# Kernel tuning notes

Measured on AMD Instinct MI355X. Metric: run time of the kernel, lower is better.

The kernel has to match this reference:

```python
import jax, jax.numpy as jnp
import numpy as np

D = 256   # hidden_dim
N = 1024  # total nodes
NP = 384  # paratope nodes
NE = 384  # epitope nodes
NC = 14   # atom channels


def setup_inputs() -> dict:
    key = jax.random.key(0)
    ks = jax.random.split(key, 24)
    s = 1.0 / np.sqrt(D)
    s3 = 1.0 / np.sqrt(3 * D)
    w = lambda k, shape, sc: (jax.random.normal(k, shape, jnp.float32) * sc)
    z = lambda: jnp.zeros((D,), jnp.float32)
    return {
        "H": w(ks[0], (N, D), 1.0),
        "X": w(ks[1], (N, NC, 3), 1.0),
        "paratope_mask": jnp.zeros((N,), bool).at[:NP].set(True),
        "epitope_mask": jnp.zeros((N,), bool).at[NP:NP + NE].set(True),
        "res_w1": w(ks[2], (1, D), 1.0), "res_b1": z(),
        "res_w2": w(ks[3], (D, D), s), "res_b2": z(),
        "atom_w1": w(ks[4], (1, D), 1.0), "atom_b1": z(),
        "atom_w2": w(ks[5], (D, D), s), "atom_b2": z(),
        "sim_weight": jnp.float32(0.5),
        "int_w1": w(ks[6], (3 * D, D), s3), "int_b1": z(),
        "int_w2": w(ks[7], (D, D), s), "int_b2": z(),
        "wl": w(ks[8], (D, D), s),
        "wr": w(ks[9], (D, D), s),
        "wg_w": w(ks[10], (D, D), s), "wg_b": z(),
        "wq_w": w(ks[11], (D, D), s), "wq_b": z(),
        "wk_w": w(ks[12], (D, D), s), "wk_b": z(),
        "wv_w": w(ks[13], (D, D), s), "wv_b": z(),
    }


def _mlp2(x, w1, b1, w2, b2):
    return jax.nn.silu(x @ w1 + b1) @ w2 + b2


def reference(H, X, paratope_mask, epitope_mask,
              res_w1, res_b1, res_w2, res_b2,
              atom_w1, atom_b1, atom_w2, atom_b2,
              sim_weight,
              int_w1, int_b1, int_w2, int_b2,
              wl, wr, wg_w, wg_b, wq_w, wq_b, wk_w, wk_b, wv_w, wv_b):
    p_idx = jnp.nonzero(paratope_mask, size=NP)[0]
    e_idx = jnp.nonzero(epitope_mask, size=NE)[0]
    Hp = H[p_idx]                      # [NP, D]
    He = H[e_idx]                      # [NE, D]
    Xp_ca = X[p_idx, 1]                # [NP, 3] (CA atom)
    Xe_ca = X[e_idx, 1]                # [NE, 3]

    dX = Xp_ca[:, None, :] - Xe_ca[None, :, :]         # [NP, NE, 3]
    S = jnp.sum(dX * dX, axis=-1, keepdims=True)       # [NP, NE, 1]
    # original computes S_residue and S_atom with identical formula
    S_res = _mlp2(S, res_w1, res_b1, res_w2, res_b2)
    S_atom = _mlp2(S, atom_w1, atom_b1, atom_w2, atom_b2)
    wmix = jax.nn.sigmoid(sim_weight)
    S_comb = wmix * S_res + (1.0 - wmix) * S_atom      # [NP, NE, D]

    Hp_e = jnp.broadcast_to(Hp[:, None, :], (NP, NE, D))
    He_e = jnp.broadcast_to(He[None, :, :], (NP, NE, D))
    Z_in = jnp.concatenate([Hp_e, He_e, S_comb], axis=-1)  # [NP, NE, 3D]
    Z = _mlp2(Z_in, int_w1, int_b1, int_w2, int_b2)        # [NP, NE, D]

    I = (Hp @ wl)[:, None, :] * (He @ wr)[None, :, :]      # outer-product interaction
    gate = jax.nn.sigmoid(Z @ wg_w + wg_b)
    f_tri = gate * I

    Q = Z @ wq_w + wq_b
    K = Z @ wk_w + wk_b
    V = Z @ wv_w + wv_b
    scores = jnp.einsum('ped,pfd->pef', Q, K) / (D ** 0.5)  # [NP, NE, NE]
    A = jax.nn.softmax(scores, axis=-1)
    f_att = jnp.einsum('pef,pfd->ped', A, V)

    H_tri = f_tri + f_att                                   # [NP, NE, D]
    return H.at[p_idx].set(H_tri.mean(axis=1))
```

## Files before the change

### kernel.cpp

```cpp
#include <hip/hip_runtime.h>

#define NPAR 384
#define NEPI 384
#define DD   256
#define NTAB 4096
#define SMAX 96.0f
#define SDELTA (SMAX / NTAB)
#define SINVD (NTAB / SMAX)

using bf16x8 = __bf16 __attribute__((ext_vector_type(8)));
using bf16x2 = __bf16 __attribute__((ext_vector_type(2)));
using f32x4  = float __attribute__((ext_vector_type(4)));

#if defined(__has_builtin)
#if __has_builtin(__builtin_amdgcn_cvt_pk_bf16_f32)
#define HAVE_PK_BF16 1
#endif
#endif

__device__ __forceinline__ float sigm(float x) { return 1.0f / (1.0f + __expf(-x)); }
__device__ __forceinline__ float silu(float x) { return x / (1.0f + __expf(-x)); }
__device__ __forceinline__ unsigned short f2bf(float f) {
  unsigned u = __float_as_uint(f);
  u += 0x7fffu + ((u >> 16) & 1u);
  return (unsigned short)(u >> 16);
}
__device__ __forceinline__ float bf2f(unsigned u16) {
  return __uint_as_float(u16 << 16);
}
__device__ __forceinline__ float bf2f_lo(unsigned w) {
  return __uint_as_float(w << 16);
}
__device__ __forceinline__ float bf2f_hi(unsigned w) {
  return __uint_as_float(w & 0xffff0000u);
}
__device__ __forceinline__ uint2 pack4(float a, float b, float c, float d) {
  uint2 r;
#ifdef HAVE_PK_BF16
  bf16x2 lo = __builtin_amdgcn_cvt_pk_bf16_f32(a, b);
  bf16x2 hi = __builtin_amdgcn_cvt_pk_bf16_f32(c, d);
  r.x = __builtin_bit_cast(unsigned, lo);
  r.y = __builtin_bit_cast(unsigned, hi);
#else
  r.x = (unsigned)f2bf(a) | ((unsigned)f2bf(b) << 16);
  r.y = (unsigned)f2bf(c) | ((unsigned)f2bf(d) << 16);
#endif
  return r;
}


__global__ void prep_kernel(
    const float* __restrict__ H, const float* __restrict__ wl,
    const float* __restrict__ wr, const float* __restrict__ int_w1,
    const float* __restrict__ res_w2, const float* __restrict__ atom_w2,
    const float* __restrict__ res_b2, const float* __restrict__ atom_b2,
    const float* __restrict__ int_b1, const float* __restrict__ simw,
    const float* __restrict__ wq_b, const float* __restrict__ wk_w,
    const float* __restrict__ wq_w,
    float* __restrict__ Hpl, float* __restrict__ Her,
    float* __restrict__ P1, float* __restrict__ P2,
    float* __restrict__ MrF, float* __restrict__ MaF,
    float* __restrict__ cvec, float* __restrict__ gv,
    float* __restrict__ WqkF) {
  __shared__ float sbuf[1024];
  const int b = blockIdx.x, t = threadIdx.x;
  if (b < 256) {
    const bool isMa = b >= 128;
    const int i0 = (b & 127) * 2;
    const float wmix = 1.0f / (1.0f + __expf(-simw[0]));
    const float sc = isMa ? (1.0f - wmix) : wmix;
    const float* W2 = isMa ? atom_w2 : res_w2;
    sbuf[t] = W2[i0 * 256 + t];
    sbuf[256 + t] = W2[(i0 + 1) * 256 + t];
    __syncthreads();
    float a0 = 0.f, a1 = 0.f;
#pragma unroll 8
    for (int k = 0; k < 256; ++k) {
      const float w = int_w1[(512 + k) * 256 + t];
      a0 = fmaf(sbuf[k], w, a0);
      a1 = fmaf(sbuf[256 + k], w, a1);
    }
    float* dst = isMa ? MaF : MrF;
    dst[i0 * 256 + t] = a0 * sc;
    dst[(i0 + 1) * 256 + t] = a1 * sc;
  } else if (b == 256) {
    const float wmix = 1.0f / (1.0f + __expf(-simw[0]));
    float acc = int_b1[t];
#pragma unroll 8
    for (int k = 0; k < 256; ++k) {
      float bm = wmix * res_b2[k] + (1.0f - wmix) * atom_b2[k];
      acc += bm * int_w1[(512 + k) * 256 + t];
    }
    cvec[t] = acc;
  } else if (b < 321) {
    const int lane = t & 63, w = t >> 6;
    const int d = (b - 257) * 4 + w;
    float acc = 0.f;
#pragma unroll
    for (int i = 0; i < 4; ++i) {
      const int c = i * 64 + lane;
      acc += wk_w[d * 256 + c] * wq_b[c];
    }
    acc += __shfl_xor(acc, 1);
    acc += __shfl_xor(acc, 2);
    acc += __shfl_xor(acc, 4);
    acc += __shfl_xor(acc, 8);
    acc += __shfl_xor(acc, 16);
    acc += __shfl_xor(acc, 32);
    if (lane == 0) gv[d] = acc;
  } else if (b < 577) {
    const int r = b - 321;
    sbuf[t] = wq_w[r * 256 + t];
    __syncthreads();
    const float* wkrow = wk_w + t * 256;
    float a0 = 0.f, a1 = 0.f, a2 = 0.f, a3 = 0.f;
#pragma unroll 4
    for (int k = 0; k < 256; k += 4) {
      const f32x4 wv4 = *reinterpret_cast<const f32x4*>(&wkrow[k]);
      a0 = fmaf(sbuf[k + 0], wv4[0], a0);
      a1 = fmaf(sbuf[k + 1], wv4[1], a1);
      a2 = fmaf(sbuf[k + 2], wv4[2], a2);
      a3 = fmaf(sbuf[k + 3], wv4[3], a3);
    }
    WqkF[r * 256 + t] = (a0 + a1) + (a2 + a3);
  } else {
    const int idx = b - 577;
    const int seg = idx / 96, r0 = (idx % 96) * 4;
    const float* A;
    const float* B;
    float* C;
    switch (seg) {
      case 0:  A = H + r0 * 256;            B = wl;              C = Hpl + r0 * 256; break;
      case 1:  A = H + (NPAR + r0) * 256;   B = wr;              C = Her + r0 * 256; break;
      case 2:  A = H + r0 * 256;            B = int_w1;          C = P1 + r0 * 256;  break;
      default: A = H + (NPAR + r0) * 256;   B = int_w1 + 65536;  C = P2 + r0 * 256;  break;
    }
#pragma unroll
    for (int j = 0; j < 4; ++j) sbuf[j * 256 + t] = A[j * 256 + t];
    __syncthreads();
    float a0 = 0.f, a1 = 0.f, a2 = 0.f, a3 = 0.f;
#pragma unroll 8
    for (int k = 0; k < 256; ++k) {
      const float bv = B[k * 256 + t];
      a0 = fmaf(sbuf[k], bv, a0);
      a1 = fmaf(sbuf[256 + k], bv, a1);
      a2 = fmaf(sbuf[512 + k], bv, a2);
      a3 = fmaf(sbuf[768 + k], bv, a3);
    }
    C[t] = a0;
    C[256 + t] = a1;
    C[512 + t] = a2;
    C[768 + t] = a3;
  }
}

__global__ void pack_kernel(const float* __restrict__ MrF, const float* __restrict__ MaF,
                            const float* __restrict__ w2, const float* __restrict__ wg,
                            const float* __restrict__ WqkF, unsigned short* __restrict__ wpack) {
  const int idx = blockIdx.x * 256 + threadIdx.x;
  const int m = idx >> 16;
  const int r = idx & 65535;
  const int chunk = r >> 9;
  const int lane = (r >> 3) & 63;
  const int j = r & 7;
  const int k = (chunk >> 4) * 32 + (lane >> 4) * 8 + j;
  const int n = (chunk & 15) * 16 + (lane & 15);
  const float* src;
  switch (m) {
    case 0: src = MrF; break;
    case 1: src = MaF; break;
    case 2: src = w2; break;
    case 3: src = wg; break;
    default: src = WqkF; break;
  }
  wpack[idx] = f2bf(src[k * 256 + n]);
}


__device__ __forceinline__ void zero_acc4(f32x4 (&acc)[4][4]) {
#pragma unroll
  for (int mt = 0; mt < 4; ++mt)
#pragma unroll
    for (int nt = 0; nt < 4; ++nt)
      acc[mt][nt] = (f32x4){0.f, 0.f, 0.f, 0.f};
}

__device__ __forceinline__ void gemm4(f32x4 (&acc)[4][4],
                                      const unsigned short* __restrict__ wp,
                                      const unsigned short* ub, int lane, int wv) {
  const int l15 = lane & 15, l4 = lane >> 4;
#pragma unroll
  for (int ks = 0; ks < 8; ++ks) {
    bf16x8 a[4];
#pragma unroll
    for (int mt = 0; mt < 4; ++mt)
      a[mt] = *reinterpret_cast<const bf16x8*>(wp + ((ks * 16 + wv * 4 + mt) * 64 + lane) * 8);
#pragma unroll
    for (int nt = 0; nt < 4; ++nt) {
      bf16x8 b = *reinterpret_cast<const bf16x8*>(ub + (nt * 16 + l15) * 264 + ks * 32 + l4 * 8);
#pragma unroll
      for (int mt = 0; mt < 4; ++mt)
        acc[mt][nt] = __builtin_amdgcn_mfma_f32_16x16x32_bf16(a[mt], b, acc[mt][nt], 0, 0, 0);
    }
  }
}

__device__ __forceinline__ void fill_u(unsigned short* ub, const float* Sv,
                                       const float* __restrict__ w1,
                                       const float* __restrict__ b1, int t) {
  const int dg = t & 31, rb = t >> 5;
  const f32x4 w1a = *reinterpret_cast<const f32x4*>(&w1[dg * 8]);
  const f32x4 w1b = *reinterpret_cast<const f32x4*>(&w1[dg * 8 + 4]);
  const f32x4 b1a = *reinterpret_cast<const f32x4*>(&b1[dg * 8]);
  const f32x4 b1b = *reinterpret_cast<const f32x4*>(&b1[dg * 8 + 4]);
#pragma unroll
  for (int i = 0; i < 8; ++i) {
    const int e = rb + i * 8;
    const float s = Sv[e];
    uint2 lo = pack4(silu(fmaf(s, w1a[0], b1a[0])), silu(fmaf(s, w1a[1], b1a[1])),
                     silu(fmaf(s, w1a[2], b1a[2])), silu(fmaf(s, w1a[3], b1a[3])));
    uint2 hi = pack4(silu(fmaf(s, w1b[0], b1b[0])), silu(fmaf(s, w1b[1], b1b[1])),
                     silu(fmaf(s, w1b[2], b1b[2])), silu(fmaf(s, w1b[3], b1b[3])));
    uint4 pk = {lo.x, lo.y, hi.x, hi.y};
    *reinterpret_cast<uint4*>(&ub[e * 264 + dg * 8]) = pk;
  }
}


__global__ __launch_bounds__(256, 3) void tab_kernel(
    const float* __restrict__ res_w1, const float* __restrict__ res_b1,
    const float* __restrict__ atom_w1, const float* __restrict__ atom_b1,
    const unsigned short* __restrict__ wpack, unsigned short* __restrict__ tab) {
  __shared__ __align__(16) unsigned short ubuf[64 * 264];
  __shared__ float Sv[64];
  const int t = threadIdx.x, lane = t & 63, wv = t >> 6;
  const int l15 = lane & 15, l4 = lane >> 4;
  const int n0 = blockIdx.x * 64;
  if (t < 64) Sv[t] = (n0 + t) * SDELTA;
  __syncthreads();
  f32x4 acc[4][4];
  zero_acc4(acc);
  fill_u(ubuf, Sv, res_w1, res_b1, t);
  __syncthreads();
  gemm4(acc, wpack + 0 * 65536, ubuf, lane, wv);
  __syncthreads();
  fill_u(ubuf, Sv, atom_w1, atom_b1, t);
  __syncthreads();
  gemm4(acc, wpack + 1 * 65536, ubuf, lane, wv);
#pragma unroll
  for (int mt = 0; mt < 4; ++mt) {
    const int d = wv * 64 + mt * 16 + l4 * 4;
#pragma unroll
    for (int nt = 0; nt < 4; ++nt) {
      const int n = n0 + nt * 16 + l15;
      *reinterpret_cast<uint2*>(&tab[n * 256 + d]) =
          pack4(acc[mt][nt][0], acc[mt][nt][1], acc[mt][nt][2], acc[mt][nt][3]);
    }
  }
}


__global__ __launch_bounds__(256, 4) void pair_kernel(
    const float* __restrict__ Xg, const unsigned short* __restrict__ tab,
    const float* __restrict__ int_b2, const float* __restrict__ wg_b,
    const unsigned short* __restrict__ wpack, const float* __restrict__ cvec,
    const float* __restrict__ P1, const float* __restrict__ P2,
    const float* __restrict__ Hpl, const float* __restrict__ Her,
    float* __restrict__ ftri, unsigned short* __restrict__ Zsw) {
  __shared__ __align__(16) unsigned short ubuf[64 * 264];
  __shared__ float Sv[64];
  __shared__ float pc[DD];
  const int t = threadIdx.x, lane = t & 63, wv = t >> 6;
  const int l15 = lane & 15, l4 = lane >> 4;
  const int p = blockIdx.x / 6, cc = blockIdx.x % 6, e0 = cc * 64;
  const int d0 = wv * 64;

  if (t < 64) {
    const int e = e0 + t;
    float dx = Xg[p * 42 + 3] - Xg[(NPAR + e) * 42 + 3];
    float dy = Xg[p * 42 + 4] - Xg[(NPAR + e) * 42 + 4];
    float dz = Xg[p * 42 + 5] - Xg[(NPAR + e) * 42 + 5];
    Sv[t] = dx * dx + dy * dy + dz * dz;
  }
  pc[t] = P1[p * DD + t] + cvec[t];
  __syncthreads();

  {
    const int dg = t & 31, rb = t >> 5;
    const f32x4 pca = *reinterpret_cast<const f32x4*>(&pc[dg * 8]);
    const f32x4 pcb = *reinterpret_cast<const f32x4*>(&pc[dg * 8 + 4]);
#pragma unroll
    for (int i = 0; i < 8; ++i) {
      const int e = rb + i * 8;
      float sv = Sv[e] * SINVD;
      int idx = (int)sv;
      idx = idx > (NTAB - 2) ? (NTAB - 2) : idx;
      const float fr = sv - (float)idx;
      const uint4 t0 = *reinterpret_cast<const uint4*>(&tab[idx * 256 + dg * 8]);
      const uint4 t1 = *reinterpret_cast<const uint4*>(&tab[(idx + 1) * 256 + dg * 8]);
      const f32x4 p2a = *reinterpret_cast<const f32x4*>(&P2[(e0 + e) * DD + dg * 8]);
      const f32x4 p2b = *reinterpret_cast<const f32x4*>(&P2[(e0 + e) * DD + dg * 8 + 4]);
      float z0 = bf2f_lo(t0.x), z1 = bf2f_hi(t0.x), z2 = bf2f_lo(t0.y), z3 = bf2f_hi(t0.y);
      float z4 = bf2f_lo(t0.z), z5 = bf2f_hi(t0.z), z6 = bf2f_lo(t0.w), z7 = bf2f_hi(t0.w);
      z0 = fmaf(fr, bf2f_lo(t1.x) - z0, z0) + pca[0] + p2a[0];
      z1 = fmaf(fr, bf2f_hi(t1.x) - z1, z1) + pca[1] + p2a[1];
      z2 = fmaf(fr, bf2f_lo(t1.y) - z2, z2) + pca[2] + p2a[2];
      z3 = fmaf(fr, bf2f_hi(t1.y) - z3, z3) + pca[3] + p2a[3];
      z4 = fmaf(fr, bf2f_lo(t1.z) - z4, z4) + pcb[0] + p2b[0];
      z5 = fmaf(fr, bf2f_hi(t1.z) - z5, z5) + pcb[1] + p2b[1];
      z6 = fmaf(fr, bf2f_lo(t1.w) - z6, z6) + pcb[2] + p2b[2];
      z7 = fmaf(fr, bf2f_hi(t1.w) - z7, z7) + pcb[3] + p2b[3];
      uint2 lo = pack4(silu(z0), silu(z1), silu(z2), silu(z3));
      uint2 hi = pack4(silu(z4), silu(z5), silu(z6), silu(z7));
      uint4 pk = {lo.x, lo.y, hi.x, hi.y};
      *reinterpret_cast<uint4*>(&ubuf[e * 264 + dg * 8]) = pk;
    }
  }
  __syncthreads();

  f32x4 acc[4][4];
  zero_acc4(acc);
  gemm4(acc, wpack + 2 * 65536, ubuf, lane, wv);
  __syncthreads();
#pragma unroll
  for (int mt = 0; mt < 4; ++mt) {
    const int d = d0 + mt * 16 + l4 * 4;
    const f32x4 bb = *reinterpret_cast<const f32x4*>(&int_b2[d]);
#pragma unroll
    for (int nt = 0; nt < 4; ++nt) {
      const int e = nt * 16 + l15;
      *reinterpret_cast<uint2*>(&ubuf[e * 264 + d]) =
          pack4(acc[mt][nt][0] + bb[0], acc[mt][nt][1] + bb[1],
                acc[mt][nt][2] + bb[2], acc[mt][nt][3] + bb[3]);
    }
  }
  __syncthreads();

  {
    unsigned short* Zd = Zsw + (size_t)p * 98304 + (size_t)(cc * 4 + wv) * 4096 + lane * 8;
#pragma unroll
    for (int ks = 0; ks < 8; ++ks) {
      *reinterpret_cast<uint4*>(Zd + ks * 512) =
          *reinterpret_cast<const uint4*>(&ubuf[(wv * 16 + l15) * 264 + ks * 32 + l4 * 8]);
    }
  }

  zero_acc4(acc);
  gemm4(acc, wpack + 3 * 65536, ubuf, lane, wv);
#pragma unroll
  for (int mt = 0; mt < 4; ++mt) {
    const int d = d0 + mt * 16 + l4 * 4;
    const f32x4 bb = *reinterpret_cast<const f32x4*>(&wg_b[d]);
    const f32x4 hl = *reinterpret_cast<const f32x4*>(&Hpl[p * DD + d]);
    f32x4 fs = (f32x4){0.f, 0.f, 0.f, 0.f};
#pragma unroll
    for (int nt = 0; nt < 4; ++nt) {
      const int e = e0 + nt * 16 + l15;
      const f32x4 hr = *reinterpret_cast<const f32x4*>(&Her[e * DD + d]);
#pragma unroll
      for (int r = 0; r < 4; ++r)
        fs[r] += sigm(acc[mt][nt][r] + bb[r]) * hr[r];
    }
#pragma unroll
    for (int r = 0; r < 4; ++r) {
      float v = fs[r] * hl[r];
      v += __shfl_xor(v, 1);
      v += __shfl_xor(v, 2);
      v += __shfl_xor(v, 4);
      v += __shfl_xor(v, 8);
      if (l15 == 0) atomicAdd(&ftri[p * DD + d + r], v);
    }
  }
}


__global__ __launch_bounds__(256, 4) void attn_kernel(
    const unsigned short* __restrict__ Zsw, const float* __restrict__ gv,
    const unsigned short* __restrict__ wpack, float* __restrict__ cbufg) {
  __shared__ __align__(16) unsigned short Tc[32 * 264];
  __shared__ float red[128];
  __shared__ float red2[128];
  const int t = threadIdx.x, lane = t & 63, wv = t >> 6;
  const int l15 = lane & 15, l4 = lane >> 4;
  const int xcd = blockIdx.x & 7, inner = blockIdx.x >> 3;
  const int p = (inner / 12) * 8 + xcd, c = inner % 12;
  const unsigned short* Zsp = Zsw + (size_t)p * 98304;
  const unsigned short* wqk = wpack + 4 * 65536;

  {
    f32x4 ta[4][2];
#pragma unroll
    for (int mt = 0; mt < 4; ++mt)
#pragma unroll
      for (int nt = 0; nt < 2; ++nt) ta[mt][nt] = (f32x4){0.f, 0.f, 0.f, 0.f};
    const unsigned short* Tb = Zsp + (size_t)(c * 2) * 4096 + lane * 8;
    bf16x8 bcur[2], bnxt[2];
#pragma unroll
    for (int nt = 0; nt < 2; ++nt)
      bcur[nt] = *reinterpret_cast<const bf16x8*>(Tb + nt * 4096);
#pragma unroll
    for (int ks = 0; ks < 8; ++ks) {
      if (ks < 7) {
#pragma unroll
        for (int nt = 0; nt < 2; ++nt)
          bnxt[nt] = *reinterpret_cast<const bf16x8*>(Tb + nt * 4096 + (ks + 1) * 512);
      }
      bf16x8 a[4];
#pragma unroll
      for (int mt = 0; mt < 4; ++mt)
        a[mt] = *reinterpret_cast<const bf16x8*>(wqk + ((ks * 16 + wv * 4 + mt) * 64 + lane) * 8);
#pragma unroll
      for (int nt = 0; nt < 2; ++nt)
#pragma unroll
        for (int mt = 0; mt < 4; ++mt)
          ta[mt][nt] = __builtin_amdgcn_mfma_f32_16x16x32_bf16(a[mt], bcur[nt], ta[mt][nt], 0, 0, 0);
      if (ks < 7) {
#pragma unroll
        for (int nt = 0; nt < 2; ++nt) bcur[nt] = bnxt[nt];
      }
    }
#pragma unroll
    for (int mt = 0; mt < 4; ++mt) {
      const int d = wv * 64 + mt * 16 + l4 * 4;
      const f32x4 gq = *reinterpret_cast<const f32x4*>(&gv[d]);
#pragma unroll
      for (int nt = 0; nt < 2; ++nt) {
        const int e = nt * 16 + l15;
        *reinterpret_cast<uint2*>(&Tc[e * 264 + d]) =
            pack4((ta[mt][nt][0] + gq[0]) * 0.0625f, (ta[mt][nt][1] + gq[1]) * 0.0625f,
                  (ta[mt][nt][2] + gq[2]) * 0.0625f, (ta[mt][nt][3] + gq[3]) * 0.0625f);
      }
    }
  }
  __syncthreads();

  f32x4 sc[2][6];
#pragma unroll
  for (int mt = 0; mt < 2; ++mt)
#pragma unroll
    for (int s = 0; s < 6; ++s) sc[mt][s] = (f32x4){0.f, 0.f, 0.f, 0.f};

  {
    const unsigned short* Sb = Zsp + (size_t)wv * 4096 + lane * 8;
    bf16x8 b0[3], b1[3];
#pragma unroll
    for (int j = 0; j < 3; ++j)
      b0[j] = *reinterpret_cast<const bf16x8*>(Sb + j * 16384);
#pragma unroll
    for (int ks = 0; ks < 8; ++ks) {
#pragma unroll
      for (int j = 0; j < 3; ++j)
        b1[j] = *reinterpret_cast<const bf16x8*>(Sb + (3 + j) * 16384 + ks * 512);
      bf16x8 a[2];
#pragma unroll
      for (int mt = 0; mt < 2; ++mt)
        a[mt] = *reinterpret_cast<const bf16x8*>(&Tc[(mt * 16 + l15) * 264 + ks * 32 + l4 * 8]);
#pragma unroll
      for (int j = 0; j < 3; ++j)
#pragma unroll
        for (int mt = 0; mt < 2; ++mt)
          sc[mt][j] = __builtin_amdgcn_mfma_f32_16x16x32_bf16(a[mt], b0[j], sc[mt][j], 0, 0, 0);
      if (ks < 7) {
#pragma unroll
        for (int j = 0; j < 3; ++j)
          b0[j] = *reinterpret_cast<const bf16x8*>(Sb + j * 16384 + (ks + 1) * 512);
      }
#pragma unroll
      for (int j = 0; j < 3; ++j)
#pragma unroll
        for (int mt = 0; mt < 2; ++mt)
          sc[mt][3 + j] = __builtin_amdgcn_mfma_f32_16x16x32_bf16(a[mt], b1[j], sc[mt][3 + j], 0, 0, 0);
    }
  }

  float rmax[2][4];
#pragma unroll
  for (int mt = 0; mt < 2; ++mt) {
#pragma unroll
    for (int r = 0; r < 4; ++r) {
      float m = -1e30f;
#pragma unroll
      for (int s = 0; s < 6; ++s) m = fmaxf(m, sc[mt][s][r]);
      m = fmaxf(m, __shfl_xor(m, 1));
      m = fmaxf(m, __shfl_xor(m, 2));
      m = fmaxf(m, __shfl_xor(m, 4));
      m = fmaxf(m, __shfl_xor(m, 8));
      rmax[mt][r] = m;
    }
  }
  if (l15 == 0) {
#pragma unroll
    for (int mt = 0; mt < 2; ++mt)
#pragma unroll
      for (int r = 0; r < 4; ++r)
        red[wv * 32 + mt * 16 + l4 * 4 + r] = rmax[mt][r];
  }
  __syncthreads();
#pragma unroll
  for (int mt = 0; mt < 2; ++mt) {
#pragma unroll
    for (int r = 0; r < 4; ++r) {
      const int row = mt * 16 + l4 * 4 + r;
      rmax[mt][r] = fmaxf(fmaxf(red[row], red[32 + row]), fmaxf(red[64 + row], red[96 + row]));
    }
  }

  float rsum[2][4];
#pragma unroll
  for (int mt = 0; mt < 2; ++mt) {
#pragma unroll
    for (int r = 0; r < 4; ++r) {
      float sSum = 0.f;
#pragma unroll
      for (int s = 0; s < 6; ++s) {
        float e = __expf(sc[mt][s][r] - rmax[mt][r]);
        sc[mt][s][r] = e;
        sSum += e;
      }
      sSum += __shfl_xor(sSum, 1);
      sSum += __shfl_xor(sSum, 2);
      sSum += __shfl_xor(sSum, 4);
      sSum += __shfl_xor(sSum, 8);
      rsum[mt][r] = sSum;
    }
  }
  if (l15 == 0) {
#pragma unroll
    for (int mt = 0; mt < 2; ++mt)
#pragma unroll
      for (int r = 0; r < 4; ++r)
        red2[wv * 32 + mt * 16 + l4 * 4 + r] = rsum[mt][r];
  }
  __syncthreads();
  float rinv[2][4];
#pragma unroll
  for (int mt = 0; mt < 2; ++mt) {
#pragma unroll
    for (int r = 0; r < 4; ++r) {
      const int row = mt * 16 + l4 * 4 + r;
      rinv[mt][r] = 1.0f / (red2[row] + red2[32 + row] + red2[64 + row] + red2[96 + row]);
    }
  }

#pragma unroll
  for (int s = 0; s < 6; ++s) {
    float v = 0.f;
#pragma unroll
    for (int mt = 0; mt < 2; ++mt)
#pragma unroll
      for (int r = 0; r < 4; ++r)
        v += sc[mt][s][r] * rinv[mt][r];
    v += __shfl_xor(v, 16);
    v += __shfl_xor(v, 32);
    if (lane < 16)
      atomicAdd(&cbufg[p * NEPI + (s * 4 + wv) * 16 + lane], v);
  }
}


__global__ __launch_bounds__(256) void outa_kernel(
    const unsigned short* __restrict__ Zsw, const float* __restrict__ cbufg,
    float* __restrict__ ubufg) {
  __shared__ float cb[128];
  __shared__ float part[16][257];
  const int p = blockIdx.x / 3, th = blockIdx.x % 3, g0 = th * 8;
  const int t = threadIdx.x;
  const int lane = t & 63, wv = t >> 6;
  const int l15 = lane & 15, l4 = lane >> 4;
  if (t < 128) cb[t] = cbufg[p * NEPI + g0 * 16 + t];
  __syncthreads();
  const unsigned short* Zsp = Zsw + (size_t)p * 98304;
  float a16[16];
#pragma unroll
  for (int j = 0; j < 16; ++j) a16[j] = 0.f;
#pragma unroll
  for (int gr = 0; gr < 8; ++gr) {
    const int grp = g0 + gr;
    const float w = cb[gr * 16 + l15];
    const uint4 z0 = *reinterpret_cast<const uint4*>(Zsp + grp * 4096 + wv * 512 + lane * 8);
    const uint4 z1 = *reinterpret_cast<const uint4*>(Zsp + grp * 4096 + (wv + 4) * 512 + lane * 8);
    a16[0] = fmaf(w, bf2f(z0.x & 0xffffu), a16[0]);
    a16[1] = fmaf(w, bf2f(z0.x >> 16), a16[1]);
    a16[2] = fmaf(w, bf2f(z0.y & 0xffffu), a16[2]);
    a16[3] = fmaf(w, bf2f(z0.y >> 16), a16[3]);
    a16[4] = fmaf(w, bf2f(z0.z & 0xffffu), a16[4]);
    a16[5] = fmaf(w, bf2f(z0.z >> 16), a16[5]);
    a16[6] = fmaf(w, bf2f(z0.w & 0xffffu), a16[6]);
    a16[7] = fmaf(w, bf2f(z0.w >> 16), a16[7]);
    a16[8]  = fmaf(w, bf2f(z1.x & 0xffffu), a16[8]);
    a16[9]  = fmaf(w, bf2f(z1.x >> 16), a16[9]);
    a16[10] = fmaf(w, bf2f(z1.y & 0xffffu), a16[10]);
    a16[11] = fmaf(w, bf2f(z1.y >> 16), a16[11]);
    a16[12] = fmaf(w, bf2f(z1.z & 0xffffu), a16[12]);
    a16[13] = fmaf(w, bf2f(z1.z >> 16), a16[13]);
    a16[14] = fmaf(w, bf2f(z1.w & 0xffffu), a16[14]);
    a16[15] = fmaf(w, bf2f(z1.w >> 16), a16[15]);
  }
#pragma unroll
  for (int j = 0; j < 8; ++j) part[l15][wv * 32 + l4 * 8 + j] = a16[j];
#pragma unroll
  for (int j = 0; j < 8; ++j) part[l15][128 + wv * 32 + l4 * 8 + j] = a16[8 + j];
  __syncthreads();
  float uu = 0.f;
#pragma unroll
  for (int g = 0; g < 16; ++g) uu += part[g][t];
  atomicAdd(&ubufg[p * DD + t], uu);
}


__global__ __launch_bounds__(256) void out2_kernel(
    const float* __restrict__ ubufg, const float* __restrict__ ftri,
    const float* __restrict__ wvw, const float* __restrict__ wvb,
    float* __restrict__ out) {
  __shared__ float u[DD];
  const int p = blockIdx.x, t = threadIdx.x;
  u[t] = ubufg[p * DD + t];
  __syncthreads();
  float acc = ftri[p * DD + t] + 384.0f * wvb[t];
#pragma unroll 8
  for (int d = 0; d < DD; ++d)
    acc = fmaf(u[d], wvw[d * DD + t], acc);
  out[p * DD + t] = acc * (1.0f / 384.0f);
}


extern "C" void kernel_launch(void* const* d_in, const int* in_sizes, int n_in,
                              void* d_out, int out_size, void* d_ws, size_t ws_size,
                              hipStream_t stream) {
  (void)in_sizes; (void)n_in; (void)out_size; (void)ws_size;
  const float* H = (const float*)d_in[0];
  const float* X = (const float*)d_in[1];
  const float* res_w1 = (const float*)d_in[4];
  const float* res_b1 = (const float*)d_in[5];
  const float* res_w2 = (const float*)d_in[6];
  const float* res_b2 = (const float*)d_in[7];
  const float* atom_w1 = (const float*)d_in[8];
  const float* atom_b1 = (const float*)d_in[9];
  const float* atom_w2 = (const float*)d_in[10];
  const float* atom_b2 = (const float*)d_in[11];
  const float* simw = (const float*)d_in[12];
  const float* int_w1 = (const float*)d_in[13];
  const float* int_b1 = (const float*)d_in[14];
  const float* int_w2 = (const float*)d_in[15];
  const float* int_b2 = (const float*)d_in[16];
  const float* wl = (const float*)d_in[17];
  const float* wr = (const float*)d_in[18];
  const float* wg_w = (const float*)d_in[19];
  const float* wg_b = (const float*)d_in[20];
  const float* wq_w = (const float*)d_in[21];
  const float* wq_b = (const float*)d_in[22];
  const float* wk_w = (const float*)d_in[23];
  const float* wv_w = (const float*)d_in[25];
  const float* wv_b = (const float*)d_in[26];

  char* ws = (char*)d_ws;
  unsigned short* wpack = (unsigned short*)(ws + 0);
  float* MrF   = (float*)(ws + 655360);
  float* MaF   = (float*)(ws + 917504);
  float* WqkF  = (float*)(ws + 1179648);
  float* cvec  = (float*)(ws + 1441792);
  float* gv    = (float*)(ws + 1442816);
  float* P1    = (float*)(ws + 1443840);
  float* P2    = (float*)(ws + 1837056);
  float* Hpl   = (float*)(ws + 2230272);
  float* Her   = (float*)(ws + 2623488);
  float* ftri  = (float*)(ws + 3016704);
  float* cbufg = (float*)(ws + 3409920);
  float* ubufg = (float*)(ws + 3999744);
  unsigned short* Zsw = (unsigned short*)(ws + 4392960);
  unsigned short* tab = (unsigned short*)(ws + 79890432);

  hipMemsetAsync(ftri, 0, 393216 + 589824 + 393216, stream);
  prep_kernel<<<961, 256, 0, stream>>>(H, wl, wr, int_w1, res_w2, atom_w2,
                                       res_b2, atom_b2, int_b1, simw, wq_b, wk_w, wq_w,
                                       Hpl, Her, P1, P2, MrF, MaF, cvec, gv, WqkF);
  pack_kernel<<<1280, 256, 0, stream>>>(MrF, MaF, int_w2, wg_w, WqkF, wpack);
  tab_kernel<<<NTAB / 64, 256, 0, stream>>>(res_w1, res_b1, atom_w1, atom_b1, wpack, tab);
  pair_kernel<<<2304, 256, 0, stream>>>(X, tab, int_b2, wg_b, wpack, cvec,
                                        P1, P2, Hpl, Her, ftri, Zsw);
  attn_kernel<<<4608, 256, 0, stream>>>(Zsw, gv, wpack, cbufg);
  outa_kernel<<<1152, 256, 0, stream>>>(Zsw, cbufg, ubufg);
  out2_kernel<<<384, 256, 0, stream>>>(ubufg, ftri, wv_w, wv_b, (float*)d_out);
  hipMemcpyAsync((float*)d_out + NPAR * DD, H + NPAR * DD,
                 (1024 - NPAR) * DD * sizeof(float), hipMemcpyDeviceToDevice, stream);
}
```

Baseline: 335.4 us.

## Fold weight packing into prep kernel and keep S lookup table in fp32

Removes the separate pack_kernel. prep_kernel now writes the fused MLP weight products straight into the bf16 MFMA-packed layout, and extra blocks pack int_w2 and wg_w. This saves one launch and the fp32 intermediate round trip. The S lookup table is now stored in fp32 rather than bf16, which doubles the table bytes read in pair_kernel in exchange for accuracy and dropping the bf16 unpack work. The scattered 2-byte stores in prep may be poorly coalesced.

```diff
diff --git a/kernel.cpp b/kernel.cpp
--- a/kernel.cpp
+++ b/kernel.cpp
@@ -27,12 +27,6 @@
 }
 __device__ __forceinline__ float bf2f(unsigned u16) {
   return __uint_as_float(u16 << 16);
-}
-__device__ __forceinline__ float bf2f_lo(unsigned w) {
-  return __uint_as_float(w << 16);
-}
-__device__ __forceinline__ float bf2f_hi(unsigned w) {
-  return __uint_as_float(w & 0xffff0000u);
 }
 __device__ __forceinline__ uint2 pack4(float a, float b, float c, float d) {
   uint2 r;
@@ -48,6 +42,14 @@
   return r;
 }
 
+__device__ __forceinline__ void store_packed(unsigned short* __restrict__ wp,
+                                             int slot, int k, int n, float v) {
+  const int ks = k >> 5, lhi = (k >> 3) & 3, j = k & 7;
+  const int tile = n >> 4, llo = n & 15;
+  const int lane = lhi * 16 + llo;
+  wp[slot * 65536 + (((ks * 16 + tile) * 64 + lane) << 3) + j] = f2bf(v);
+}
+
 
 __global__ void prep_kernel(
     const float* __restrict__ H, const float* __restrict__ wl,
@@ -56,12 +58,12 @@
     const float* __restrict__ res_b2, const float* __restrict__ atom_b2,
     const float* __restrict__ int_b1, const float* __restrict__ simw,
     const float* __restrict__ wq_b, const float* __restrict__ wk_w,
-    const float* __restrict__ wq_w,
+    const float* __restrict__ wq_w, const float* __restrict__ int_w2,
+    const float* __restrict__ wg_w,
     float* __restrict__ Hpl, float* __restrict__ Her,
     float* __restrict__ P1, float* __restrict__ P2,
-    float* __restrict__ MrF, float* __restrict__ MaF,
     float* __restrict__ cvec, float* __restrict__ gv,
-    float* __restrict__ WqkF) {
+    unsigned short* __restrict__ wpack) {
   __shared__ float sbuf[1024];
   const int b = blockIdx.x, t = threadIdx.x;
   if (b < 256) {
@@ -80,9 +82,9 @@
       a0 = fmaf(sbuf[k], w, a0);
       a1 = fmaf(sbuf[256 + k], w, a1);
     }
-    float* dst = isMa ? MaF : MrF;
-    dst[i0 * 256 + t] = a0 * sc;
-    dst[(i0 + 1) * 256 + t] = a1 * sc;
+    const int slot = isMa ? 1 : 0;
+    store_packed(wpack, slot, i0, t, a0 * sc);
+    store_packed(wpack, slot, i0 + 1, t, a1 * sc);
   } else if (b == 256) {
     const float wmix = 1.0f / (1.0f + __expf(-simw[0]));
     float acc = int_b1[t];
@@ -122,8 +124,8 @@
       a2 = fmaf(sbuf[k + 2], wv4[2], a2);
       a3 = fmaf(sbuf[k + 3], wv4[3], a3);
     }
-    WqkF[r * 256 + t] = (a0 + a1) + (a2 + a3);
-  } else {
+    store_packed(wpack, 4, r, t, (a0 + a1) + (a2 + a3));
+  } else if (b < 961) {
     const int idx = b - 577;
     const int seg = idx / 96, r0 = (idx % 96) * 4;
     const float* A;
@@ -151,29 +153,18 @@
     C[256 + t] = a1;
     C[512 + t] = a2;
     C[768 + t] = a3;
-  }
-}
-
-__global__ void pack_kernel(const float* __restrict__ MrF, const float* __restrict__ MaF,
-                            const float* __restrict__ w2, const float* __restrict__ wg,
-                            const float* __restrict__ WqkF, unsigned short* __restrict__ wpack) {
-  const int idx = blockIdx.x * 256 + threadIdx.x;
-  const int m = idx >> 16;
-  const int r = idx & 65535;
-  const int chunk = r >> 9;
-  const int lane = (r >> 3) & 63;
-  const int j = r & 7;
-  const int k = (chunk >> 4) * 32 + (lane >> 4) * 8 + j;
-  const int n = (chunk & 15) * 16 + (lane & 15);
-  const float* src;
-  switch (m) {
-    case 0: src = MrF; break;
-    case 1: src = MaF; break;
-    case 2: src = w2; break;
-    case 3: src = wg; break;
-    default: src = WqkF; break;
-  }
-  wpack[idx] = f2bf(src[k * 256 + n]);
+  } else {
+    const int idx = (b - 961) * 256 + t;
+    const int m = idx >> 16;
+    const int r = idx & 65535;
+    const int chunk = r >> 9;
+    const int lane = (r >> 3) & 63;
+    const int j = r & 7;
+    const int k = (chunk >> 4) * 32 + (lane >> 4) * 8 + j;
+    const int n = (chunk & 15) * 16 + (lane & 15);
+    const float* src = (m == 0) ? int_w2 : wg_w;
+    wpack[(2 + m) * 65536 + r] = f2bf(src[k * 256 + n]);
+  }
 }
 
 
@@ -230,7 +221,7 @@
 __global__ __launch_bounds__(256, 3) void tab_kernel(
     const float* __restrict__ res_w1, const float* __restrict__ res_b1,
     const float* __restrict__ atom_w1, const float* __restrict__ atom_b1,
-    const unsigned short* __restrict__ wpack, unsigned short* __restrict__ tab) {
+    const unsigned short* __restrict__ wpack, float* __restrict__ tabF) {
   __shared__ __align__(16) unsigned short ubuf[64 * 264];
   __shared__ float Sv[64];
   const int t = threadIdx.x, lane = t & 63, wv = t >> 6;
@@ -253,15 +244,14 @@
 #pragma unroll
     for (int nt = 0; nt < 4; ++nt) {
       const int n = n0 + nt * 16 + l15;
-      *reinterpret_cast<uint2*>(&tab[n * 256 + d]) =
-          pack4(acc[mt][nt][0], acc[mt][nt][1], acc[mt][nt][2], acc[mt][nt][3]);
+      *reinterpret_cast<f32x4*>(&tabF[n * 256 + d]) = acc[mt][nt];
     }
   }
 }
 
 
 __global__ __launch_bounds__(256, 4) void pair_kernel(
-    const float* __restrict__ Xg, const unsigned short* __restrict__ tab,
+    const float* __restrict__ Xg, const float* __restrict__ tabF,
     const float* __restrict__ int_b2, const float* __restrict__ wg_b,
     const unsigned short* __restrict__ wpack, const float* __restrict__ cvec,
     const float* __restrict__ P1, const float* __restrict__ P2,
@@ -296,20 +286,20 @@
       int idx = (int)sv;
       idx = idx > (NTAB - 2) ? (NTAB - 2) : idx;
       const float fr = sv - (float)idx;
-      const uint4 t0 = *reinterpret_cast<const uint4*>(&tab[idx * 256 + dg * 8]);
-      const uint4 t1 = *reinterpret_cast<const uint4*>(&tab[(idx + 1) * 256 + dg * 8]);
+      const f32x4 t0a = *reinterpret_cast<const f32x4*>(&tabF[idx * 256 + dg * 8]);
+      const f32x4 t0b = *reinterpret_cast<const f32x4*>(&tabF[idx * 256 + dg * 8 + 4]);
+      const f32x4 t1a = *reinterpret_cast<const f32x4*>(&tabF[(idx + 1) * 256 + dg * 8]);
+      const f32x4 t1b = *reinterpret_cast<const f32x4*>(&tabF[(idx + 1) * 256 + dg * 8 + 4]);
       const f32x4 p2a = *reinterpret_cast<const f32x4*>(&P2[(e0 + e) * DD + dg * 8]);
       const f32x4 p2b = *reinterpret_cast<const f32x4*>(&P2[(e0 + e) * DD + dg * 8 + 4]);
-      float z0 = bf2f_lo(t0.x), z1 = bf2f_hi(t0.x), z2 = bf2f_lo(t0.y), z3 = bf2f_hi(t0.y);
-      float z4 = bf2f_lo(t0.z), z5 = bf2f_hi(t0.z), z6 = bf2f_lo(t0.w), z7 = bf2f_hi(t0.w);
-      z0 = fmaf(fr, bf2f_lo(t1.x) - z0, z0) + pca[0] + p2a[0];
-      z1 = fmaf(fr, bf2f_hi(t1.x) - z1, z1) + pca[1] + p2a[1];
-      z2 = fmaf(fr, bf2f_lo(t1.y) - z2, z2) + pca[2] + p2a[2];
-      z3 = fmaf(fr, bf2f_hi(t1.y) - z3, z3) + pca[3] + p2a[3];
-      z4 = fmaf(fr, bf2f_lo(t1.z) - z4, z4) + pcb[0] + p2b[0];
-      z5 = fmaf(fr, bf2f_hi(t1.z) - z5, z5) + pcb[1] + p2b[1];
-      z6 = fmaf(fr, bf2f_lo(t1.w) - z6, z6) + pcb[2] + p2b[2];
-      z7 = fmaf(fr, bf2f_hi(t1.w) - z7, z7) + pcb[3] + p2b[3];
+      float z0 = fmaf(fr, t1a[0] - t0a[0], t0a[0]) + pca[0] + p2a[0];
+      float z1 = fmaf(fr, t1a[1] - t0a[1], t0a[1]) + pca[1] + p2a[1];
+      float z2 = fmaf(fr, t1a[2] - t0a[2], t0a[2]) + pca[2] + p2a[2];
+      float z3 = fmaf(fr, t1a[3] - t0a[3], t0a[3]) + pca[3] + p2a[3];
+      float z4 = fmaf(fr, t1b[0] - t0b[0], t0b[0]) + pcb[0] + p2b[0];
+      float z5 = fmaf(fr, t1b[1] - t0b[1], t0b[1]) + pcb[1] + p2b[1];
+      float z6 = fmaf(fr, t1b[2] - t0b[2], t0b[2]) + pcb[2] + p2b[2];
+      float z7 = fmaf(fr, t1b[3] - t0b[3], t0b[3]) + pcb[3] + p2b[3];
       uint2 lo = pack4(silu(z0), silu(z1), silu(z2), silu(z3));
       uint2 hi = pack4(silu(z4), silu(z5), silu(z6), silu(z7));
       uint4 pk = {lo.x, lo.y, hi.x, hi.y};
@@ -655,28 +645,25 @@
 
   char* ws = (char*)d_ws;
   unsigned short* wpack = (unsigned short*)(ws + 0);
-  float* MrF   = (float*)(ws + 655360);
-  float* MaF   = (float*)(ws + 917504);
-  float* WqkF  = (float*)(ws + 1179648);
-  float* cvec  = (float*)(ws + 1441792);
-  float* gv    = (float*)(ws + 1442816);
-  float* P1    = (float*)(ws + 1443840);
-  float* P2    = (float*)(ws + 1837056);
-  float* Hpl   = (float*)(ws + 2230272);
-  float* Her   = (float*)(ws + 2623488);
-  float* ftri  = (float*)(ws + 3016704);
-  float* cbufg = (float*)(ws + 3409920);
-  float* ubufg = (float*)(ws + 3999744);
-  unsigned short* Zsw = (unsigned short*)(ws + 4392960);
-  unsigned short* tab = (unsigned short*)(ws + 79890432);
+  float* cvec  = (float*)(ws + 655360);
+  float* gv    = (float*)(ws + 656384);
+  float* P1    = (float*)(ws + 657408);
+  float* P2    = (float*)(ws + 1050624);
+  float* Hpl   = (float*)(ws + 1443840);
+  float* Her   = (float*)(ws + 1837056);
+  float* ftri  = (float*)(ws + 2230272);
+  float* cbufg = (float*)(ws + 2623488);
+  float* ubufg = (float*)(ws + 3213312);
+  unsigned short* Zsw = (unsigned short*)(ws + 3606528);
+  float* tabF  = (float*)(ws + 79104000);
 
   hipMemsetAsync(ftri, 0, 393216 + 589824 + 393216, stream);
-  prep_kernel<<<961, 256, 0, stream>>>(H, wl, wr, int_w1, res_w2, atom_w2,
-                                       res_b2, atom_b2, int_b1, simw, wq_b, wk_w, wq_w,
-                                       Hpl, Her, P1, P2, MrF, MaF, cvec, gv, WqkF);
-  pack_kernel<<<1280, 256, 0, stream>>>(MrF, MaF, int_w2, wg_w, WqkF, wpack);
-  tab_kernel<<<NTAB / 64, 256, 0, stream>>>(res_w1, res_b1, atom_w1, atom_b1, wpack, tab);
-  pair_kernel<<<2304, 256, 0, stream>>>(X, tab, int_b2, wg_b, wpack, cvec,
+  prep_kernel<<<1473, 256, 0, stream>>>(H, wl, wr, int_w1, res_w2, atom_w2,
+                                        res_b2, atom_b2, int_b1, simw, wq_b, wk_w,
+                                        wq_w, int_w2, wg_w,
+                                        Hpl, Her, P1, P2, cvec, gv, wpack);
+  tab_kernel<<<NTAB / 64, 256, 0, stream>>>(res_w1, res_b1, atom_w1, atom_b1, wpack, tabF);
+  pair_kernel<<<2304, 256, 0, stream>>>(X, tabF, int_b2, wg_b, wpack, cvec,
                                         P1, P2, Hpl, Her, ftri, Zsw);
   attn_kernel<<<4608, 256, 0, stream>>>(Zsw, gv, wpack, cbufg);
   outa_kernel<<<1152, 256, 0, stream>>>(Zsw, cbufg, ubufg);
```

Result: faster. 328.2 us (-2.1%).
